# Kernel optimization log

Measured on AMD Instinct MI355X. Metric: run time of the kernel, lower is better.

## Reference

```python
import jax, jax.numpy as jnp
import numpy as np

RADIUS = 0.4   # 0.2 * nlayer, nlayer = 2
NSAMPLE = 32   # k


def _fps(xyz, m):
    """Farthest point sampling. xyz: (B, N, 3) -> idx (B, m) int32.
    Matches pointnet2 CUDA kernel: first sampled point is index 0."""
    B, N, _ = xyz.shape

    def step(carry, _):
        dist, far = carry
        centroid = jnp.take_along_axis(xyz, far[:, None, None], axis=1)  # (B,1,3)
        d = jnp.sum((xyz - centroid) ** 2, axis=-1)                      # (B,N)
        dist = jnp.minimum(dist, d)
        return (dist, jnp.argmax(dist, axis=-1).astype(jnp.int32)), far

    init = (jnp.full((B, N), jnp.inf, dtype=xyz.dtype),
            jnp.zeros((B,), dtype=jnp.int32))
    _, idx = jax.lax.scan(step, init, None, length=m)  # (m, B)
    return idx.T                                       # (B, m)


def _ball_query(radius, k, xyz, new_xyz):
    """xyz (B,N,3), new_xyz (B,M,3) -> (B,M,k) int32.
    First k in-radius indices in ascending index order; slots past the
    number of in-radius points are filled with the first found index
    (pointnet2 ball_query semantics)."""
    N = xyz.shape[1]
    d2 = jnp.sum((new_xyz[:, :, None, :] - xyz[:, None, :, :]) ** 2, axis=-1)  # (B,M,N)
    key = jnp.where(d2 < radius * radius,
                    jnp.arange(N, dtype=jnp.int32), jnp.int32(N))              # (B,M,N)
    topv, _ = jax.lax.top_k(-key, k)   # k smallest keys, ascending
    idx = -topv                        # (B,M,k)
    valid = idx < N
    idx = jnp.where(valid, idx, idx[..., :1])  # pad with first found index
    return idx


def _group(t, idx):
    """t (B,C,N), idx (B,M,k) -> (B,C,M,k)."""
    return jnp.take_along_axis(t[:, :, None, :], idx[:, None, :, :], axis=3)


def setup_inputs() -> dict:
    key = jax.random.key(0)
    k1, k2, k3 = jax.random.split(key, 3)
    return {
        "x": jax.random.normal(k1, (8, 3, 8192), dtype=jnp.float32),
        "feature": jax.random.normal(k2, (8, 64, 8192), dtype=jnp.float32),
        "weight": jax.random.normal(k3, (64, 64), dtype=jnp.float32) / 8.0,
        "num_pool": 2048,
    }


def reference(x, feature, weight, num_pool):
    # x: (B,3,N) coordinates, feature: (B,C,N), weight: 1x1 conv (C_out, C_in)
    xyz = jnp.transpose(x, (0, 2, 1))                       # (B,N,3)
    fps_idx = _fps(xyz, num_pool)                           # (B,M)
    new_xyz = jnp.take_along_axis(xyz, fps_idx[:, :, None], axis=1)  # (B,M,3)
    sub_idx = _ball_query(RADIUS, NSAMPLE, xyz, new_xyz)    # (B,M,k)

    x_out = _group(x, sub_idx).max(axis=-1)                 # (B,3,M)
    fg = _group(feature, sub_idx)                           # (B,C,M,k)
    f_out = jnp.einsum('oc,bcmk->bomk', weight, fg).max(axis=-1)  # (B,C,M)
    return x_out, f_out
```

## Files before the change

kernel.cpp:

```cpp
#include <hip/hip_runtime.h>
#include <cstdint>
#include <cstddef>

#define BB 8
#define NN 8192
#define CC 64
#define MM 2048
#define KK 32

typedef float vfloat2 __attribute__((ext_vector_type(2)));

__device__ __forceinline__ float sqdist_exact(float x, float y, float z,
                                              float cx, float cy, float cz) {
    float dx = __fsub_rn(x, cx);
    float dy = __fsub_rn(y, cy);
    float dz = __fsub_rn(z, cz);
    return __fadd_rn(__fadd_rn(__fmul_rn(dx, dx), __fmul_rn(dy, dy)),
                     __fmul_rn(dz, dz));
}

template <int CTRL>
__device__ __forceinline__ unsigned long long dpp_max_u64(unsigned long long key) {
    int lo = (int)(unsigned)key;
    int hi = (int)(unsigned)(key >> 32);
    int slo = __builtin_amdgcn_update_dpp(0, lo, CTRL, 0xF, 0xF, true);
    int shi = __builtin_amdgcn_update_dpp(0, hi, CTRL, 0xF, 0xF, true);
    unsigned long long o = ((unsigned long long)(unsigned)shi << 32) | (unsigned)slo;
    return o > key ? o : key;
}

__global__ __launch_bounds__(512) void fps_kernel(const float* __restrict__ x,
                                                  int* __restrict__ fps_idx) {
#pragma clang fp contract(off)
    const int b = blockIdx.x;
    const int tid = threadIdx.x;
    const int lane = tid & 63;
    const int wv = tid >> 6;
    const float* xb = x + (size_t)b * 3 * NN;
    int* fps_store = fps_idx + b * MM;

    __shared__ float sx[NN];
    __shared__ float sy[NN];
    __shared__ float sz[NN];
    __shared__ unsigned long long red2[2][8];

    const vfloat2* gx = (const vfloat2*)xb;
    const vfloat2* gy = (const vfloat2*)(xb + NN);
    const vfloat2* gz = (const vfloat2*)(xb + 2 * NN);

    vfloat2 px[8], py[8], pz[8], dist[8];
#pragma unroll
    for (int p = 0; p < 8; ++p) {
        const int e = tid + p * 512;
        px[p] = gx[e];
        py[p] = gy[e];
        pz[p] = gz[e];
        ((vfloat2*)sx)[e] = px[p];
        ((vfloat2*)sy)[e] = py[p];
        ((vfloat2*)sz)[e] = pz[p];
        dist[p] = (vfloat2){INFINITY, INFINITY};
    }
    __syncthreads();

    int far = 0;
    for (int t = 0; t < MM; ++t) {
        if (tid == 0) fps_store[t] = far;
        const float cx = sx[far];
        const float cy = sy[far];
        const float cz = sz[far];
        const vfloat2 cx2 = {cx, cx};
        const vfloat2 cy2 = {cy, cy};
        const vfloat2 cz2 = {cz, cz};

        float maxv = -1.0f;
#pragma unroll
        for (int p = 0; p < 8; ++p) {
            vfloat2 dx = px[p] - cx2;
            vfloat2 dy = py[p] - cy2;
            vfloat2 dz = pz[p] - cz2;
            vfloat2 m1 = dx * dx;
            vfloat2 m2 = dy * dy;
            vfloat2 m3 = dz * dz;
            vfloat2 s = (m1 + m2) + m3;
            vfloat2 nd;
            nd.x = fminf(dist[p].x, s.x);
            nd.y = fminf(dist[p].y, s.y);
            dist[p] = nd;
            maxv = fmaxf(fmaxf(maxv, nd.x), nd.y);
        }
        int maxi = 0;
#pragma unroll
        for (int p = 7; p >= 0; --p) {
            const int i0 = 2 * (tid + p * 512);
            if (dist[p].y == maxv) maxi = i0 + 1;
            if (dist[p].x == maxv) maxi = i0;
        }
        unsigned long long key =
            ((unsigned long long)__float_as_uint(maxv) << 32) | (unsigned)(~(unsigned)maxi);
        key = dpp_max_u64<0x111>(key);
        key = dpp_max_u64<0x112>(key);
        key = dpp_max_u64<0x114>(key);
        key = dpp_max_u64<0x118>(key);
        key = dpp_max_u64<0x142>(key);
        key = dpp_max_u64<0x143>(key);
        if (lane == 63) red2[t & 1][wv] = key;
        __syncthreads();
        unsigned long long best = red2[t & 1][0];
#pragma unroll
        for (int j = 1; j < 8; ++j) {
            unsigned long long o2 = red2[t & 1][j];
            if (o2 > best) best = o2;
        }
        far = (int)(~(unsigned)best);
    }
}

__global__ __launch_bounds__(256) void transform_kernel(const float* __restrict__ feature,
                                                        const float* __restrict__ weight,
                                                        float* __restrict__ g) {
    __shared__ float Wl[64 * 64];
    const int tid = threadIdx.x;
    for (int k = tid; k < 64 * 64; k += 256) Wl[k] = weight[k];
    __syncthreads();

    const int P = blockIdx.x * 256 + tid;
    const int b = P >> 13;
    const int n = P & (NN - 1);
    const float* fb = feature + (size_t)b * CC * NN + n;

    float fr[64];
#pragma unroll
    for (int c = 0; c < 64; ++c) fr[c] = fb[(size_t)c * NN];

    float* go = g + ((size_t)b << 19) + (size_t)n * 64;
    for (int o = 0; o < 64; o += 4) {
        const float* w0 = &Wl[o * 64];
        const float* w1 = w0 + 64;
        const float* w2 = w0 + 128;
        const float* w3 = w0 + 192;
        float a0 = 0.f, a1 = 0.f, a2 = 0.f, a3 = 0.f;
#pragma unroll
        for (int c = 0; c < 64; c += 4) {
            float4 v0 = *(const float4*)(w0 + c);
            float4 v1 = *(const float4*)(w1 + c);
            float4 v2 = *(const float4*)(w2 + c);
            float4 v3 = *(const float4*)(w3 + c);
            a0 += v0.x * fr[c] + v0.y * fr[c + 1] + v0.z * fr[c + 2] + v0.w * fr[c + 3];
            a1 += v1.x * fr[c] + v1.y * fr[c + 1] + v1.z * fr[c + 2] + v1.w * fr[c + 3];
            a2 += v2.x * fr[c] + v2.y * fr[c + 1] + v2.z * fr[c + 2] + v2.w * fr[c + 3];
            a3 += v3.x * fr[c] + v3.y * fr[c + 1] + v3.z * fr[c + 2] + v3.w * fr[c + 3];
        }
        float4 r;
        r.x = a0; r.y = a1; r.z = a2; r.w = a3;
        *(float4*)(go + o) = r;
    }
}

__global__ __launch_bounds__(256) void bq_kernel(const float* __restrict__ x,
                                                 const int* __restrict__ fps_idx,
                                                 int* __restrict__ sub_idx,
                                                 float* __restrict__ xout) {
    const float R2 = (float)(0.4 * 0.4);
    int gw = (int)((blockIdx.x * 256 + threadIdx.x) >> 6);
    const int lane = threadIdx.x & 63;
    gw = __builtin_amdgcn_readfirstlane(gw);
    const int b = gw >> 11;
    const int m = gw & (MM - 1);
    const float* xb = x + (size_t)b * 3 * NN;

    const int ctr = fps_idx[gw];
    const float cx = xb[ctr];
    const float cy = xb[NN + ctr];
    const float cz = xb[2 * NN + ctr];

    int* sid = sub_idx + (size_t)gw * KK;
    int found = 0;
    int first = 0;
    float mx = -INFINITY, my = -INFINITY, mz = -INFINITY;

    for (int base = 0; base < NN; base += 64) {
        const int i = base + lane;
        const float xx = xb[i];
        const float yy = xb[NN + i];
        const float zz = xb[2 * NN + i];
        const float d2 = sqdist_exact(xx, yy, zz, cx, cy, cz);
        const bool q = d2 < R2;
        const unsigned long long mask = __ballot(q);
        if (q) {
            int pos = found + (int)__popcll(mask & ((1ull << lane) - 1ull));
            if (pos < KK) {
                sid[pos] = i;
                mx = fmaxf(mx, xx);
                my = fmaxf(my, yy);
                mz = fmaxf(mz, zz);
            }
        }
        if (found == 0 && mask != 0ull) first = base + (int)__builtin_ctzll(mask);
        found += (int)__popcll(mask);
        if (found >= KK) break;
    }
    if (found < KK) {
        if (lane < KK - found) sid[found + lane] = first;
    }
#pragma unroll
    for (int off = 32; off >= 1; off >>= 1) {
        mx = fmaxf(mx, __shfl_xor(mx, off, 64));
        my = fmaxf(my, __shfl_xor(my, off, 64));
        mz = fmaxf(mz, __shfl_xor(mz, off, 64));
    }
    if (lane == 0) {
        xout[(size_t)b * 3 * MM + 0 * MM + m] = mx;
        xout[(size_t)b * 3 * MM + 1 * MM + m] = my;
        xout[(size_t)b * 3 * MM + 2 * MM + m] = mz;
    }
}

__global__ __launch_bounds__(256) void gather_kernel(const float* __restrict__ g,
                                                     const int* __restrict__ sub_idx,
                                                     float* __restrict__ fout) {
    int gw = (int)((blockIdx.x * 256 + threadIdx.x) >> 6);
    const int lane = threadIdx.x & 63;
    gw = __builtin_amdgcn_readfirstlane(gw);
    const int b = gw >> 11;
    const int m = gw & (MM - 1);
    const int* sid = sub_idx + (size_t)gw * KK;
    const float* gb = g + ((size_t)b << 19);
    float acc = -INFINITY;
#pragma unroll
    for (int j = 0; j < KK; ++j) {
        const int id = sid[j];
        acc = fmaxf(acc, gb[(size_t)id * 64 + lane]);
    }
    fout[((size_t)b << 17) + ((size_t)lane << 11) + m] = acc;
}

extern "C" void kernel_launch(void* const* d_in, const int* in_sizes, int n_in,
                              void* d_out, int out_size, void* d_ws, size_t ws_size,
                              hipStream_t stream) {
    const float* x = (const float*)d_in[0];
    const float* feature = (const float*)d_in[1];
    const float* weight = (const float*)d_in[2];

    float* out = (float*)d_out;
    float* xout = out;
    float* fout = out + BB * 3 * MM;

    char* ws = (char*)d_ws;
    int* fps_idx = (int*)ws;
    int* sub_idx = (int*)(ws + (size_t)BB * MM * 4);
    float* g = (float*)(ws + (size_t)BB * MM * 4 + (size_t)BB * MM * KK * 4);

    fps_kernel<<<BB, 512, 0, stream>>>(x, fps_idx);
    transform_kernel<<<(BB * NN) / 256, 256, 0, stream>>>(feature, weight, g);
    bq_kernel<<<(BB * MM * 64) / 256, 256, 0, stream>>>(x, fps_idx, sub_idx, xout);
    gather_kernel<<<(BB * MM * 64) / 256, 256, 0, stream>>>(g, sub_idx, fout);
}
```

Measured before the change: 2.032 ms.

## Spatially sort FPS points into Morton bins and skip far thread clusters

Before farthest point sampling starts, points are bucketed into a 512-bin Morton grid using fixed normal-distribution octile thresholds and counting-sorted in shared memory. Each thread then owns 16 spatially clustered points and keeps their bounding box. In each iteration a thread skips its distance update when the lower bound from the box to the new centroid cannot beat its current max. This removes redundant distance work, at the cost of a sort prologue, extra shared memory and wave divergence. The bin thresholds assume roughly Gaussian coordinates but remain correct for other inputs.

```diff
diff --git a/kernel.cpp b/kernel.cpp
--- a/kernel.cpp
+++ b/kernel.cpp
@@ -27,6 +27,18 @@
     int shi = __builtin_amdgcn_update_dpp(0, hi, CTRL, 0xF, 0xF, true);
     unsigned long long o = ((unsigned long long)(unsigned)shi << 32) | (unsigned)slo;
     return o > key ? o : key;
+}
+
+__device__ __forceinline__ int octile(float v) {
+    return (v > -1.1503494f) + (v > -0.6744898f) + (v > -0.3186394f) + (v > 0.0f) +
+           (v > 0.3186394f) + (v > 0.6744898f) + (v > 1.1503494f);
+}
+
+__device__ __forceinline__ int morton9(int bx, int by, int bz) {
+    int m = (bz & 1) | ((bz & 2) << 2) | ((bz & 4) << 4);
+    m |= ((by & 1) << 1) | ((by & 2) << 3) | ((by & 4) << 5);
+    m |= ((bx & 1) << 2) | ((bx & 2) << 4) | ((bx & 4) << 6);
+    return m;
 }
 
 __global__ __launch_bounds__(512) void fps_kernel(const float* __restrict__ x,
@@ -42,61 +54,118 @@
     __shared__ float sx[NN];
     __shared__ float sy[NN];
     __shared__ float sz[NN];
+    __shared__ int sidx[NN];
+    __shared__ int hist[512];
+    __shared__ int scanb[512];
     __shared__ unsigned long long red2[2][8];
 
     const vfloat2* gx = (const vfloat2*)xb;
     const vfloat2* gy = (const vfloat2*)(xb + NN);
     const vfloat2* gz = (const vfloat2*)(xb + 2 * NN);
 
-    vfloat2 px[8], py[8], pz[8], dist[8];
+    vfloat2 lx[8], ly[8], lz[8];
 #pragma unroll
     for (int p = 0; p < 8; ++p) {
         const int e = tid + p * 512;
-        px[p] = gx[e];
-        py[p] = gy[e];
-        pz[p] = gz[e];
-        ((vfloat2*)sx)[e] = px[p];
-        ((vfloat2*)sy)[e] = py[p];
-        ((vfloat2*)sz)[e] = pz[p];
-        dist[p] = (vfloat2){INFINITY, INFINITY};
-    }
-    __syncthreads();
-
+        lx[p] = gx[e];
+        ly[p] = gy[e];
+        lz[p] = gz[e];
+        ((vfloat2*)sx)[e] = lx[p];
+        ((vfloat2*)sy)[e] = ly[p];
+        ((vfloat2*)sz)[e] = lz[p];
+    }
+    hist[tid] = 0;
+    __syncthreads();
+
+    int mybin[16];
+#pragma unroll
+    for (int p = 0; p < 8; ++p) {
+        int b0 = morton9(octile(lx[p].x), octile(ly[p].x), octile(lz[p].x));
+        int b1 = morton9(octile(lx[p].y), octile(ly[p].y), octile(lz[p].y));
+        mybin[2 * p] = b0;
+        mybin[2 * p + 1] = b1;
+        atomicAdd(&hist[b0], 1);
+        atomicAdd(&hist[b1], 1);
+    }
+    __syncthreads();
+    int own = hist[tid];
+    scanb[tid] = own;
+    __syncthreads();
+    for (int off = 1; off < 512; off <<= 1) {
+        int add = (tid >= off) ? scanb[tid - off] : 0;
+        __syncthreads();
+        scanb[tid] += add;
+        __syncthreads();
+    }
+    hist[tid] = scanb[tid] - own;
+    __syncthreads();
+#pragma unroll
+    for (int p = 0; p < 8; ++p) {
+        const int i0 = 2 * (tid + p * 512);
+        int pos0 = atomicAdd(&hist[mybin[2 * p]], 1);
+        sidx[pos0] = i0;
+        int pos1 = atomicAdd(&hist[mybin[2 * p + 1]], 1);
+        sidx[pos1] = i0 + 1;
+    }
+    __syncthreads();
+
+    float px[16], py[16], pz[16], dist[16];
+    int idxr[16];
+#pragma unroll
+    for (int p = 0; p < 16; ++p) {
+        const int j = sidx[tid * 16 + p];
+        idxr[p] = j;
+        px[p] = sx[j];
+        py[p] = sy[j];
+        pz[p] = sz[j];
+        dist[p] = INFINITY;
+    }
+    float blx = px[0], bhx = px[0];
+    float bly = py[0], bhy = py[0];
+    float blz = pz[0], bhz = pz[0];
+#pragma unroll
+    for (int p = 1; p < 16; ++p) {
+        blx = fminf(blx, px[p]); bhx = fmaxf(bhx, px[p]);
+        bly = fminf(bly, py[p]); bhy = fmaxf(bhy, py[p]);
+        blz = fminf(blz, pz[p]); bhz = fmaxf(bhz, pz[p]);
+    }
+
+    float cmax = INFINITY;
+    int cidx = idxr[0];
     int far = 0;
     for (int t = 0; t < MM; ++t) {
         if (tid == 0) fps_store[t] = far;
         const float cx = sx[far];
         const float cy = sy[far];
         const float cz = sz[far];
-        const vfloat2 cx2 = {cx, cx};
-        const vfloat2 cy2 = {cy, cy};
-        const vfloat2 cz2 = {cz, cz};
-
-        float maxv = -1.0f;
-#pragma unroll
-        for (int p = 0; p < 8; ++p) {
-            vfloat2 dx = px[p] - cx2;
-            vfloat2 dy = py[p] - cy2;
-            vfloat2 dz = pz[p] - cz2;
-            vfloat2 m1 = dx * dx;
-            vfloat2 m2 = dy * dy;
-            vfloat2 m3 = dz * dz;
-            vfloat2 s = (m1 + m2) + m3;
-            vfloat2 nd;
-            nd.x = fminf(dist[p].x, s.x);
-            nd.y = fminf(dist[p].y, s.y);
-            dist[p] = nd;
-            maxv = fmaxf(fmaxf(maxv, nd.x), nd.y);
-        }
-        int maxi = 0;
-#pragma unroll
-        for (int p = 7; p >= 0; --p) {
-            const int i0 = 2 * (tid + p * 512);
-            if (dist[p].y == maxv) maxi = i0 + 1;
-            if (dist[p].x == maxv) maxi = i0;
+
+        float qx = cx - fminf(fmaxf(cx, blx), bhx);
+        float qy = cy - fminf(fmaxf(cy, bly), bhy);
+        float qz = cz - fminf(fmaxf(cz, blz), bhz);
+        float bound = (qx * qx + qy * qy) + qz * qz;
+        if (!(bound * 0.999f >= cmax)) {
+            float mv = -1.0f;
+#pragma unroll
+            for (int p = 0; p < 16; ++p) {
+                float dx = px[p] - cx;
+                float dy = py[p] - cy;
+                float dz = pz[p] - cz;
+                float s = (dx * dx + dy * dy) + dz * dz;
+                float nd = fminf(dist[p], s);
+                dist[p] = nd;
+                mv = fmaxf(mv, nd);
+            }
+            int mi = 0x7FFFFFFF;
+#pragma unroll
+            for (int p = 0; p < 16; ++p) {
+                int cand = (dist[p] == mv) ? idxr[p] : 0x7FFFFFFF;
+                mi = min(mi, cand);
+            }
+            cmax = mv;
+            cidx = mi;
         }
         unsigned long long key =
-            ((unsigned long long)__float_as_uint(maxv) << 32) | (unsigned)(~(unsigned)maxi);
+            ((unsigned long long)__float_as_uint(cmax) << 32) | (unsigned)(~(unsigned)cidx);
         key = dpp_max_u64<0x111>(key);
         key = dpp_max_u64<0x112>(key);
         key = dpp_max_u64<0x114>(key);
```

Result: no change. 2.021 ms (-0.6%).
